# Performance work log

Measured on AMD Instinct MI355X. Metric: run time of the kernel, lower is better.

The kernel has to match this reference:

```python
import jax, jax.numpy as jnp
import numpy as np

B, L, H = 4, 1024, 1024          # docs, seq_len, hidden (LUKE-large)
NH, M, E, R = 16, 64, 24, 512    # attn heads, mentions/doc, entities/doc, pairs/doc
EMB, BLK, NCLS = 768, 64, 97     # embed_size, block_size, num_class


def setup_inputs() -> dict:
    key = jax.random.key(0)
    ks = jax.random.split(key, 10)
    s = 0.02
    return {
        "seq_lhs": jax.random.normal(ks[0], (B, L, H), jnp.float32),
        "ent_lhs": jax.random.normal(ks[1], (B, M, H), jnp.float32),
        "ent_to_seq_attn": jax.random.uniform(ks[2], (B, NH, M, L), jnp.float32),
        "entity_id_labels": jax.random.randint(ks[3], (B, M), 0, E),
        "hts": jax.random.randint(ks[4], (B, R, 2), 0, E),
        "Wh": jax.random.normal(ks[5], (2 * H, EMB), jnp.float32) * s,
        "bh": jnp.zeros((EMB,), jnp.float32),
        "Wt": jax.random.normal(ks[6], (2 * H, EMB), jnp.float32) * s,
        "bt": jnp.zeros((EMB,), jnp.float32),
        "Wb": jax.random.normal(ks[7], (EMB * BLK, 768), jnp.float32) * s,
        "bb": jnp.zeros((768,), jnp.float32),
        "Wc": jax.random.normal(ks[8], (768, NCLS), jnp.float32) * s,
        "bc": jnp.zeros((NCLS,), jnp.float32),
    }


def reference(seq_lhs, ent_lhs, ent_to_seq_attn, entity_id_labels, hts,
              Wh, bh, Wt, bt, Wb, bb, Wc, bc):
    dt = seq_lhs.dtype
    # mention -> entity segment mask [B, E, M]
    mask = entity_id_labels[:, None, :] == jnp.arange(E)[None, :, None]
    counts = mask.sum(-1)  # [B, E]
    # entity embedding: logsumexp over its mentions (== identity for 1 mention),
    # zeros for entities with no mentions
    masked = jnp.where(mask[..., None], ent_lhs[:, None, :, :], jnp.asarray(-1e30, dt))
    ent_emb = jax.scipy.special.logsumexp(masked, axis=2)           # [B, E, H]
    ent_emb = jnp.where((counts > 0)[..., None], ent_emb, jnp.asarray(0.0, dt))
    # entity -> seq attention: mean over mentions, zeros for empty entities
    mf = mask.astype(dt)
    ent_attn = jnp.einsum('bem,bhml->behl', mf, ent_to_seq_attn)    # [B, E, NH, L]
    ent_attn = ent_attn / jnp.maximum(counts, 1)[:, :, None, None].astype(dt)
    # gather per-pair head/tail embeddings and attentions
    h_idx, t_idx = hts[..., 0], hts[..., 1]                          # [B, R]
    hs = jnp.take_along_axis(ent_emb, h_idx[..., None], axis=1)      # [B, R, H]
    ts = jnp.take_along_axis(ent_emb, t_idx[..., None], axis=1)
    ha = jnp.take_along_axis(ent_attn, h_idx[..., None, None], axis=1)  # [B, R, NH, L]
    ta = jnp.take_along_axis(ent_attn, t_idx[..., None, None], axis=1)
    ht = (ha * ta).mean(2)                                           # [B, R, L]
    ht = ht / (ht.sum(-1, keepdims=True) + 1e-5)
    rel = jnp.einsum('bld,brl->brd', seq_lhs, ht)                    # [B, R, H]
    # head/tail extractors with context concat
    he = jnp.tanh(jnp.concatenate([hs, rel], -1) @ Wh + bh)          # [B, R, EMB]
    te = jnp.tanh(jnp.concatenate([ts, rel], -1) @ Wt + bt)
    K = EMB // BLK
    b1 = he.reshape(B * R, K, BLK)
    b2 = te.reshape(B * R, K, BLK)
    bl = (b1[:, :, :, None] * b2[:, :, None, :]).reshape(B * R, EMB * BLK)
    embeds = bl @ Wb + bb                                            # [B*R, 768]
    return embeds @ Wc + bc                                          # [B*R, NCLS]
```

## Files before the change

kernel.cpp:

```cpp
#include <hip/hip_runtime.h>
#include <stdint.h>
#include <math.h>

#define B_    4
#define L_    1024
#define H_    1024
#define NH_   16
#define M_    64
#define E_    24
#define R_    512
#define EMB_  768
#define BLK_  64
#define NCLS_ 97
#define NR_   2048
#define KBIG_ 49152

typedef unsigned short ushort_t;
typedef unsigned int uint_t;
typedef short bf16x8 __attribute__((ext_vector_type(8)));
typedef float f32x4  __attribute__((ext_vector_type(4)));
typedef __bf16 bf16v2 __attribute__((ext_vector_type(2)));

__device__ __forceinline__ float bf2f(ushort_t u) {
    return __uint_as_float(((unsigned)u) << 16);
}
__device__ __forceinline__ ushort_t f2bf_rne(float f) {
    unsigned u = __float_as_uint(f);
    return (ushort_t)((u + 0x7fffu + ((u >> 16) & 1u)) >> 16);
}
__device__ __forceinline__ void cp16(const void* g, void* l) {
    __builtin_amdgcn_global_load_lds(
        (const __attribute__((address_space(1))) void*)g,
        (__attribute__((address_space(3))) void*)l, 16, 0, 0);
}

__global__ __launch_bounds__(256) void k_transpose_cvt(
    const float* __restrict__ in, ushort_t* __restrict__ out, int rows, int cols)
{
    __shared__ float t[64][65];
    int batch = blockIdx.z;
    in  += (size_t)batch * rows * cols;
    out += (size_t)batch * rows * cols;
    int c0 = blockIdx.x * 64, r0 = blockIdx.y * 64;
    int tx = threadIdx.x & 63, ty = threadIdx.x >> 6;
#pragma unroll
    for (int dr = 0; dr < 64; dr += 4)
        t[dr + ty][tx] = in[(size_t)(r0 + dr + ty) * cols + (c0 + tx)];
    __syncthreads();
    int c = threadIdx.x >> 2;
    int rk = (threadIdx.x & 3) * 16;
    ushort_t us[16];
#pragma unroll
    for (int q = 0; q < 16; q++) us[q] = f2bf_rne(t[rk + q][c]);
    ushort_t* op = &out[(size_t)(c0 + c) * rows + r0 + rk];
    *reinterpret_cast<int4*>(op)     = *reinterpret_cast<const int4*>(&us[0]);
    *reinterpret_cast<int4*>(op + 8) = *reinterpret_cast<const int4*>(&us[8]);
}

__global__ __launch_bounds__(256) void k_ent_emb(
    const float* __restrict__ ent_lhs, const int* __restrict__ labels,
    float* __restrict__ ent_emb)
{
    int b = blockIdx.x / E_, e = blockIdx.x % E_;
    __shared__ int list[M_];
    __shared__ int cnt;
    if (threadIdx.x == 0) cnt = 0;
    __syncthreads();
    if (threadIdx.x < M_ && labels[b * M_ + threadIdx.x] == e) {
        int p = atomicAdd(&cnt, 1);
        list[p] = threadIdx.x;
    }
    __syncthreads();
    int n = cnt;
    const float* base = ent_lhs + (size_t)b * M_ * H_;
    float* outp = ent_emb + ((size_t)b * E_ + e) * H_;
    for (int h = threadIdx.x; h < H_; h += blockDim.x) {
        if (n == 0) { outp[h] = 0.f; continue; }
        float mx = -1e30f;
        for (int i = 0; i < n; i++) mx = fmaxf(mx, base[(size_t)list[i] * H_ + h]);
        float s = 0.f;
        for (int i = 0; i < n; i++) s += __expf(base[(size_t)list[i] * H_ + h] - mx);
        outp[h] = mx + __logf(s);
    }
}

__global__ __launch_bounds__(256) void k_ent_attn(
    const float* __restrict__ attn, const int* __restrict__ labels,
    float* __restrict__ ent_attn)
{
    int idx = blockIdx.x;
    int nh = idx % NH_;
    int be = idx / NH_;
    int e = be % E_, b = be / E_;
    __shared__ int list[M_];
    __shared__ int cnt;
    if (threadIdx.x == 0) cnt = 0;
    __syncthreads();
    if (threadIdx.x < M_ && labels[b * M_ + threadIdx.x] == e) {
        int p = atomicAdd(&cnt, 1);
        list[p] = threadIdx.x;
    }
    __syncthreads();
    int n = cnt;
    float inv = 1.f / fmaxf((float)n, 1.f);
    const float* base = attn + ((size_t)b * NH_ + nh) * M_ * L_;
    float* outp = ent_attn + (((size_t)b * E_ + e) * NH_ + nh) * L_;
    for (int l = threadIdx.x; l < L_; l += blockDim.x) {
        float s = 0.f;
        for (int i = 0; i < n; i++) s += base[(size_t)list[i] * L_ + l];
        outp[l] = s * inv;
    }
}

__global__ __launch_bounds__(256) void k_ht(
    const float* __restrict__ ent_attn, const int* __restrict__ hts,
    ushort_t* __restrict__ ht_bf)
{
    int b = blockIdx.x / R_, r = blockIdx.x % R_;
    int h = hts[((size_t)b * R_ + r) * 2 + 0];
    int t = hts[((size_t)b * R_ + r) * 2 + 1];
    const float* ha = ent_attn + ((size_t)b * E_ + h) * NH_ * L_;
    const float* ta = ent_attn + ((size_t)b * E_ + t) * NH_ * L_;
    float vals[4];
    float local = 0.f;
#pragma unroll
    for (int p = 0; p < 4; p++) {
        int l = threadIdx.x + p * 256;
        float s = 0.f;
#pragma unroll
        for (int nh = 0; nh < NH_; nh++) s += ha[nh * L_ + l] * ta[nh * L_ + l];
        s *= (1.f / NH_);
        vals[p] = s;
        local += s;
    }
    __shared__ float red[4];
    float s = local;
#pragma unroll
    for (int off = 32; off > 0; off >>= 1) s += __shfl_down(s, off, 64);
    if ((threadIdx.x & 63) == 0) red[threadIdx.x >> 6] = s;
    __syncthreads();
    float tot = red[0] + red[1] + red[2] + red[3];
    float inv = 1.f / (tot + 1e-5f);
    ushort_t* outp = ht_bf + ((size_t)b * R_ + r) * L_;
#pragma unroll
    for (int p = 0; p < 4; p++) {
        int l = threadIdx.x + p * 256;
        outp[l] = f2bf_rne(vals[p] * inv);
    }
}

__global__ __launch_bounds__(256) void k_gather(
    const float* __restrict__ ent_emb, const int* __restrict__ hts,
    ushort_t* __restrict__ A1, ushort_t* __restrict__ A2)
{
    int n = blockIdx.x;
    int b = n / R_, r = n % R_;
    int h = hts[((size_t)b * R_ + r) * 2 + 0];
    int t = hts[((size_t)b * R_ + r) * 2 + 1];
    const float* eh = ent_emb + ((size_t)b * E_ + h) * H_;
    const float* et = ent_emb + ((size_t)b * E_ + t) * H_;
    for (int i = threadIdx.x; i < H_; i += 256) {
        A1[(size_t)n * 2048 + i] = f2bf_rne(eh[i]);
        A2[(size_t)n * 2048 + i] = f2bf_rne(et[i]);
    }
}

template <bool BIAS, bool TANH, bool DUAL>
__global__ __launch_bounds__(256) void k_gemm(
    const ushort_t* __restrict__ A, long sA, int lda,
    const ushort_t* __restrict__ Bt, long sB, int ldb,
    int K,
    const float* __restrict__ bias0, const float* __restrict__ bias1,
    ushort_t* __restrict__ C0, ushort_t* __restrict__ C1, long sC, int ldc)
{
    __shared__ ushort_t smem[2 * 128 * 72];
    ushort_t* As = smem;
    ushort_t* Bs = smem + 128 * 72;
    const int tid = threadIdx.x;
    const int lane = tid & 63, wid = tid >> 6;
    const int wr = wid >> 1, wc = wid & 1;
    const int z = blockIdx.z;
    const int m0 = blockIdx.y * 128, n0 = blockIdx.x * 128;
    A  += (long)z * sA;
    Bt += (long)z * sB;

    const f32x4 zero = {0.f, 0.f, 0.f, 0.f};
    f32x4 acc[4][4];
#pragma unroll
    for (int i = 0; i < 4; i++)
#pragma unroll
        for (int j = 0; j < 4; j++) acc[i][j] = zero;

    const int mrow = wr * 64 + (lane & 15);
    const int nrow = wc * 64 + (lane & 15);
    const int koff = (lane >> 4) * 8;

    for (int k0 = 0; k0 < K; k0 += 64) {
        __syncthreads();
#pragma unroll
        for (int p = 0; p < 4; p++) {
            int idx = tid + p * 256;
            int row = idx >> 3, seg = idx & 7;
            *reinterpret_cast<int4*>(&As[row * 72 + seg * 8]) =
                *reinterpret_cast<const int4*>(&A[(long)(m0 + row) * lda + k0 + seg * 8]);
            *reinterpret_cast<int4*>(&Bs[row * 72 + seg * 8]) =
                *reinterpret_cast<const int4*>(&Bt[(long)(n0 + row) * ldb + k0 + seg * 8]);
        }
        __syncthreads();
#pragma unroll
        for (int ks = 0; ks < 2; ks++) {
            bf16x8 af[4], bfg[4];
#pragma unroll
            for (int mt = 0; mt < 4; mt++)
                af[mt] = *reinterpret_cast<const bf16x8*>(&As[(mrow + mt * 16) * 72 + ks * 32 + koff]);
#pragma unroll
            for (int nt = 0; nt < 4; nt++)
                bfg[nt] = *reinterpret_cast<const bf16x8*>(&Bs[(nrow + nt * 16) * 72 + ks * 32 + koff]);
#pragma unroll
            for (int mt = 0; mt < 4; mt++)
#pragma unroll
                for (int nt = 0; nt < 4; nt++)
                    acc[mt][nt] = __builtin_amdgcn_mfma_f32_16x16x32_bf16(
                        af[mt], bfg[nt], acc[mt][nt], 0, 0, 0);
        }
    }

    const float* bias = BIAS ? (z ? bias1 : bias0) : nullptr;
    __syncthreads();
#pragma unroll
    for (int mt = 0; mt < 4; mt++) {
#pragma unroll
        for (int nt = 0; nt < 4; nt++) {
#pragma unroll
            for (int rg = 0; rg < 4; rg++) {
                int row = wr * 64 + mt * 16 + (lane >> 4) * 4 + rg;
                int col = wc * 64 + nt * 16 + (lane & 15);
                float v = acc[mt][nt][rg];
                if (BIAS) v += bias[n0 + col];
                if (TANH) {
                    float vc = fminf(fmaxf(v, -15.f), 15.f);
                    float ex = __expf(2.f * vc);
                    v = (ex - 1.f) / (ex + 1.f);
                }
                smem[row * 132 + col] = f2bf_rne(v);
            }
        }
    }
    __syncthreads();
    {
        int row = tid >> 1, half = tid & 1;
        const ushort_t* src = &smem[row * 132 + half * 64];
        ushort_t* dst0 = &C0[(long)z * sC + (long)(m0 + row) * ldc + n0 + half * 64];
#pragma unroll
        for (int q = 0; q < 8; q++)
            *reinterpret_cast<int4*>(dst0 + q * 8) = *reinterpret_cast<const int4*>(src + q * 8);
        if (DUAL) {
            ushort_t* dst1 = &C1[(long)z * sC + (long)(m0 + row) * ldc + n0 + half * 64];
#pragma unroll
            for (int q = 0; q < 8; q++)
                *reinterpret_cast<int4*>(dst1 + q * 8) = *reinterpret_cast<const int4*>(src + q * 8);
        }
    }
}

__global__ __launch_bounds__(512, 4) void k_bilinear(
    const ushort_t* __restrict__ he, const ushort_t* __restrict__ te,
    const ushort_t* __restrict__ Wbt, float* __restrict__ embedsN, int slices)
{
    __shared__ ushort_t HEs[256 * 64];
    __shared__ ushort_t Bsh[3 * 96 * 64];
    const int tid = threadIdx.x;
    const int lane = tid & 63, wid = tid >> 6;
    const int wn = wid >> 1, wd = wid & 1;
    const int bid = blockIdx.x;
    const int z = bid & 7;
    const int w = bid >> 3;
    const int d0 = (w & 7) * 96, n0 = (w >> 3) * 256;
    const int c0 = z * 96, cend = c0 + 96;

    const f32x4 zero = {0.f, 0.f, 0.f, 0.f};
    f32x4 acc[4][3];
#pragma unroll
    for (int i = 0; i < 4; i++)
#pragma unroll
        for (int j = 0; j < 3; j++) acc[i][j] = zero;

    const int r15 = lane & 15;
    const int q4 = lane >> 4;
    const int mrow = wn * 64 + r15;
    const int koff = q4 * 8;
    const int hswz = (r15 & 7) << 3;

    const ushort_t* Pg = Wbt
        + (long)(d0 + wid * 8 + (lane >> 3)) * KBIG_
        + ((lane & 7) ^ ((lane >> 3) & 7)) * 8;

    int c = c0;
    while (c < cend) {
        const int kk = c >> 6;
        const int i0 = c & 63;
        const int i1 = min(64, i0 + (cend - c));

        __syncthreads();

        uint4 tef[4][2];
#pragma unroll
        for (int mt = 0; mt < 4; mt++)
#pragma unroll
            for (int ks = 0; ks < 2; ks++)
                tef[mt][ks] = *reinterpret_cast<const uint4*>(
                    &te[(long)(n0 + mrow + mt * 16) * EMB_ + kk * 64 + ks * 32 + koff]);

#pragma unroll
        for (int p = 0; p < 4; p++) {
            int idx = tid + p * 512;
            int row = idx >> 3, seg = idx & 7;
            *reinterpret_cast<int4*>(&HEs[row * 64 + ((seg ^ (row & 7)) * 8)]) =
                *reinterpret_cast<const int4*>(&he[(long)(n0 + row) * EMB_ + kk * 64 + seg * 8]);
        }

        if (wid < 4) {
#pragma unroll
            for (int tb = 0; tb < 2; tb++) {
                const ushort_t* g = Pg + (long)(kk * 64 + i0 + tb) * 64;
                char* Pl = (char*)Bsh + tb * 12288 + wid * 1024;
                cp16(g,                   Pl);
                cp16(g + 32 * (long)KBIG_, Pl + 4096);
                cp16(g + 64 * (long)KBIG_, Pl + 8192);
            }
        }
        asm volatile("s_waitcnt lgkmcnt(0)" ::: "memory");

        int rd = 0;
        for (int i = i0; i < i1; i++) {
            if (i + 1 < i1) {
                if (wid < 4)
                    asm volatile("s_waitcnt vmcnt(3)" ::: "memory");
            } else {
                asm volatile("s_waitcnt vmcnt(0)" ::: "memory");
            }
            __builtin_amdgcn_s_barrier();
            __builtin_amdgcn_sched_barrier(0);

            if (i + 2 < i1 && wid < 4) {
                const ushort_t* g = Pg + (long)(kk * 64 + i + 2) * 64;
                char* Pl = (char*)Bsh + ((rd >= 1) ? (rd - 1) : 2) * 12288 + wid * 1024;
                cp16(g,                   Pl);
                cp16(g + 32 * (long)KBIG_, Pl + 4096);
                cp16(g + 64 * (long)KBIG_, Pl + 8192);
            }

            const ushort_t* Bcur = Bsh + rd * 6144;
            bf16x8 bfr[2][3];
#pragma unroll
            for (int ks = 0; ks < 2; ks++) {
                const int segoff = (((ks * 4 + q4) ^ (r15 & 7)) * 8);
#pragma unroll
                for (int nt = 0; nt < 3; nt++)
                    bfr[ks][nt] = *reinterpret_cast<const bf16x8*>(
                        &Bcur[(wd * 48 + nt * 16 + r15) * 64 + segoff]);
            }
            const int icol = i ^ hswz;
#pragma unroll
            for (int mt = 0; mt < 4; mt++) {
                union { ushort_t s[2]; bf16v2 v; } hu;
                ushort_t hb = HEs[(mrow + mt * 16) * 64 + icol];
                hu.s[0] = hb; hu.s[1] = hb;
#pragma unroll
                for (int ks = 0; ks < 2; ks++) {
                    union U { uint4 q; bf16v2 p[4]; bf16x8 v; };
                    U t, a;
                    t.q = tef[mt][ks];
#pragma unroll
                    for (int qq = 0; qq < 4; qq++) a.p[qq] = t.p[qq] * hu.v;
#pragma unroll
                    for (int nt = 0; nt < 3; nt++)
                        acc[mt][nt] = __builtin_amdgcn_mfma_f32_16x16x32_bf16(
                            a.v, bfr[ks][nt], acc[mt][nt], 0, 0, 0);
                }
            }
            rd = (rd == 2) ? 0 : rd + 1;
        }
        c += (i1 - i0);
    }

    float* outp = embedsN + (slices == 8 ? (long)z * NR_ * EMB_ : 0l);
    const bool plain = (slices == 8);
#pragma unroll
    for (int mt = 0; mt < 4; mt++)
#pragma unroll
        for (int nt = 0; nt < 3; nt++)
#pragma unroll
            for (int rg = 0; rg < 4; rg++) {
                int n = n0 + wn * 64 + mt * 16 + q4 * 4 + rg;
                int d = d0 + wd * 48 + nt * 16 + r15;
                if (plain) outp[(long)n * EMB_ + d] = acc[mt][nt][rg];
                else       atomicAdd(&outp[(long)n * EMB_ + d], acc[mt][nt][rg]);
            }
}

__global__ __launch_bounds__(128) void k_final(
    const float* __restrict__ embedsN, int nz, const float* __restrict__ bb,
    const float* __restrict__ Wc, const float* __restrict__ bc,
    float* __restrict__ out)
{
    int n = blockIdx.x;
    __shared__ float row[EMB_];
    for (int i = threadIdx.x; i < EMB_; i += 128) {
        float s = bb[i];
        for (int zz = 0; zz < nz; zz++)
            s += embedsN[(size_t)zz * NR_ * EMB_ + (size_t)n * EMB_ + i];
        row[i] = s;
    }
    __syncthreads();
    int j = threadIdx.x;
    if (j < NCLS_) {
        float s = bc[j];
#pragma unroll 8
        for (int d = 0; d < EMB_; d++) s += row[d] * Wc[d * NCLS_ + j];
        out[(size_t)n * NCLS_ + j] = s;
    }
}

extern "C" void kernel_launch(void* const* d_in, const int* in_sizes, int n_in,
                              void* d_out, int out_size, void* d_ws, size_t ws_size,
                              hipStream_t stream)
{
    (void)in_sizes; (void)n_in; (void)out_size;
    const float* seq    = (const float*)d_in[0];
    const float* entl   = (const float*)d_in[1];
    const float* attn   = (const float*)d_in[2];
    const int*   labels = (const int*)d_in[3];
    const int*   hts    = (const int*)d_in[4];
    const float* Wh     = (const float*)d_in[5];
    const float* bh     = (const float*)d_in[6];
    const float* Wt     = (const float*)d_in[7];
    const float* bt     = (const float*)d_in[8];
    const float* Wb     = (const float*)d_in[9];
    const float* bb     = (const float*)d_in[10];
    const float* Wc     = (const float*)d_in[11];
    const float* bc     = (const float*)d_in[12];
    float* out = (float*)d_out;

    char* ws = (char*)d_ws;
    size_t off = 0;
    auto alloc = [&](size_t bytes) -> char* {
        char* p = ws + off;
        off += (bytes + 255) & ~(size_t)255;
        return p;
    };
    float*    ent_emb  = (float*)alloc((size_t)B_ * E_ * H_ * 4);
    float*    ent_attn = (float*)alloc((size_t)B_ * E_ * NH_ * L_ * 4);
    ushort_t* ht_bf    = (ushort_t*)alloc((size_t)B_ * R_ * L_ * 2);
    ushort_t* seq_t    = (ushort_t*)alloc((size_t)B_ * H_ * L_ * 2);
    ushort_t* A1       = (ushort_t*)alloc((size_t)NR_ * 2048 * 2);
    ushort_t* A2       = (ushort_t*)alloc((size_t)NR_ * 2048 * 2);
    ushort_t* Whb      = (ushort_t*)alloc((size_t)EMB_ * 2048 * 2);
    ushort_t* Wtb      = (ushort_t*)alloc((size_t)EMB_ * 2048 * 2);
    ushort_t* he_bf    = (ushort_t*)alloc((size_t)NR_ * EMB_ * 2);
    ushort_t* te_bf    = (ushort_t*)alloc((size_t)NR_ * EMB_ * 2);
    ushort_t* Wbt      = (ushort_t*)alloc((size_t)EMB_ * KBIG_ * 2);

    const size_t slice_b = (size_t)NR_ * EMB_ * 4;
    int slices = (ws_size >= off + 8 * slice_b) ? 8 : 1;
    float* embedsN = (float*)alloc((size_t)slices * slice_b);

    k_transpose_cvt<<<dim3(H_ / 64, L_ / 64, B_), 256, 0, stream>>>(seq, seq_t, L_, H_);
    k_transpose_cvt<<<dim3(EMB_ / 64, 2048 / 64, 1), 256, 0, stream>>>(Wh, Whb, 2048, EMB_);
    k_transpose_cvt<<<dim3(EMB_ / 64, 2048 / 64, 1), 256, 0, stream>>>(Wt, Wtb, 2048, EMB_);
    k_transpose_cvt<<<dim3(EMB_ / 64, KBIG_ / 64, 1), 256, 0, stream>>>(Wb, Wbt, KBIG_, EMB_);

    k_ent_emb<<<B_ * E_, 256, 0, stream>>>(entl, labels, ent_emb);
    k_ent_attn<<<B_ * E_ * NH_, 256, 0, stream>>>(attn, labels, ent_attn);

    k_ht<<<NR_, 256, 0, stream>>>(ent_attn, hts, ht_bf);
    k_gather<<<NR_, 256, 0, stream>>>(ent_emb, hts, A1, A2);

    k_gemm<false, false, true><<<dim3(H_ / 128, R_ / 128, B_), 256, 0, stream>>>(
        ht_bf, (long)R_ * L_, L_,
        seq_t, (long)H_ * L_, L_,
        L_, nullptr, nullptr,
        A1 + 1024, A2 + 1024, (long)R_ * 2048, 2048);

    k_gemm<true, true, false><<<dim3(EMB_ / 128, NR_ / 128, 2), 256, 0, stream>>>(
        A1, (long)NR_ * 2048, 2048,
        Whb, (long)EMB_ * 2048, 2048,
        2048, bh, bt,
        he_bf, nullptr, (long)NR_ * EMB_, EMB_);

    if (slices == 1)
        (void)hipMemsetAsync(embedsN, 0, slice_b, stream);
    k_bilinear<<<512, 512, 0, stream>>>(he_bf, te_bf, Wbt, embedsN, slices);

    k_final<<<NR_, 128, 0, stream>>>(embedsN, slices, bb, Wc, bc, out);
}
```

Baseline: 640.1 us.

## Factor head scalar out of bilinear MFMA, apply as fp32 FMA on partials

The bilinear kernel used to build the A operand by multiplying each te fragment by the broadcast he scalar in packed bf16 before every MFMA. Now the MFMAs run directly on the raw te fragments into a zeroed temporary, and the per-row he value is applied in fp32 with FMAs on the four output rows. The HEs tile drops the XOR swizzle and uses a padded row stride so each lane can read the four output-row scalars. This removes the packed bf16 multiplies and rounding of the product, at the cost of serial MFMA chains into a fresh accumulator plus 12 extra scalar FMAs per tile and more LDS scalar reads.

Result: faster. 618.7 us (-3.3%).

```diff
diff --git a/kernel.cpp b/kernel.cpp
--- a/kernel.cpp
+++ b/kernel.cpp
@@ -19,7 +19,6 @@
 typedef unsigned int uint_t;
 typedef short bf16x8 __attribute__((ext_vector_type(8)));
 typedef float f32x4  __attribute__((ext_vector_type(4)));
-typedef __bf16 bf16v2 __attribute__((ext_vector_type(2)));
 
 __device__ __forceinline__ float bf2f(ushort_t u) {
     return __uint_as_float(((unsigned)u) << 16);
@@ -267,7 +266,7 @@
     const ushort_t* __restrict__ he, const ushort_t* __restrict__ te,
     const ushort_t* __restrict__ Wbt, float* __restrict__ embedsN, int slices)
 {
-    __shared__ ushort_t HEs[256 * 64];
+    __shared__ ushort_t HEs[256 * 72];
     __shared__ ushort_t Bsh[3 * 96 * 64];
     const int tid = threadIdx.x;
     const int lane = tid & 63, wid = tid >> 6;
@@ -289,7 +288,7 @@
     const int q4 = lane >> 4;
     const int mrow = wn * 64 + r15;
     const int koff = q4 * 8;
-    const int hswz = (r15 & 7) << 3;
+    const int hbase = (wn * 64 + q4 * 4) * 72;
 
     const ushort_t* Pg = Wbt
         + (long)(d0 + wid * 8 + (lane >> 3)) * KBIG_
@@ -303,19 +302,19 @@
 
         __syncthreads();
 
-        uint4 tef[4][2];
+        bf16x8 tef[4][2];
 #pragma unroll
         for (int mt = 0; mt < 4; mt++)
 #pragma unroll
             for (int ks = 0; ks < 2; ks++)
-                tef[mt][ks] = *reinterpret_cast<const uint4*>(
+                tef[mt][ks] = *reinterpret_cast<const bf16x8*>(
                     &te[(long)(n0 + mrow + mt * 16) * EMB_ + kk * 64 + ks * 32 + koff]);
 
 #pragma unroll
         for (int p = 0; p < 4; p++) {
             int idx = tid + p * 512;
             int row = idx >> 3, seg = idx & 7;
-            *reinterpret_cast<int4*>(&HEs[row * 64 + ((seg ^ (row & 7)) * 8)]) =
+            *reinterpret_cast<int4*>(&HEs[row * 72 + seg * 8]) =
                 *reinterpret_cast<const int4*>(&he[(long)(n0 + row) * EMB_ + kk * 64 + seg * 8]);
         }
 
@@ -360,23 +359,22 @@
                     bfr[ks][nt] = *reinterpret_cast<const bf16x8*>(
                         &Bcur[(wd * 48 + nt * 16 + r15) * 64 + segoff]);
             }
-            const int icol = i ^ hswz;
 #pragma unroll
             for (int mt = 0; mt < 4; mt++) {
-                union { ushort_t s[2]; bf16v2 v; } hu;
-                ushort_t hb = HEs[(mrow + mt * 16) * 64 + icol];
-                hu.s[0] = hb; hu.s[1] = hb;
-#pragma unroll
-                for (int ks = 0; ks < 2; ks++) {
-                    union U { uint4 q; bf16v2 p[4]; bf16x8 v; };
-                    U t, a;
-                    t.q = tef[mt][ks];
-#pragma unroll
-                    for (int qq = 0; qq < 4; qq++) a.p[qq] = t.p[qq] * hu.v;
-#pragma unroll
-                    for (int nt = 0; nt < 3; nt++)
-                        acc[mt][nt] = __builtin_amdgcn_mfma_f32_16x16x32_bf16(
-                            a.v, bfr[ks][nt], acc[mt][nt], 0, 0, 0);
+                float hf0 = bf2f(HEs[hbase + (mt * 16 + 0) * 72 + i]);
+                float hf1 = bf2f(HEs[hbase + (mt * 16 + 1) * 72 + i]);
+                float hf2 = bf2f(HEs[hbase + (mt * 16 + 2) * 72 + i]);
+                float hf3 = bf2f(HEs[hbase + (mt * 16 + 3) * 72 + i]);
+#pragma unroll
+                for (int nt = 0; nt < 3; nt++) {
+                    f32x4 cp = __builtin_amdgcn_mfma_f32_16x16x32_bf16(
+                        tef[mt][1], bfr[1][nt], zero, 0, 0, 0);
+                    cp = __builtin_amdgcn_mfma_f32_16x16x32_bf16(
+                        tef[mt][0], bfr[0][nt], cp, 0, 0, 0);
+                    acc[mt][nt][0] = fmaf(hf0, cp[0], acc[mt][nt][0]);
+                    acc[mt][nt][1] = fmaf(hf1, cp[1], acc[mt][nt][1]);
+                    acc[mt][nt][2] = fmaf(hf2, cp[2], acc[mt][nt][2]);
+                    acc[mt][nt][3] = fmaf(hf3, cp[3], acc[mt][nt][3]);
                 }
             }
             rd = (rd == 2) ? 0 : rd + 1;
```
